# Optimization experiments

Measured on AMD Instinct MI355X. Metric: run time of the kernel, lower is better.

## Reference

```python
import jax, jax.numpy as jnp
import numpy as np

BETA = 0.25


def setup_inputs() -> dict:
    key = jax.random.key(0)
    k1, k2 = jax.random.split(key)
    x = jax.random.normal(k1, (4, 4096, 256), dtype=jnp.float32)
    emb = jax.random.normal(k2, (8192, 256), dtype=jnp.float32)
    return {"x": x, "emb": emb}


def reference(x, emb):
    B, C, D = x.shape
    xf = x.reshape(-1, D)  # [B*C, D]
    # squared euclidean distances (argmin-equivalent to torch.cdist p=2)
    # dist2[i, n] = ||xf_i||^2 - 2 xf_i . e_n + ||e_n||^2
    dist2 = (
        jnp.sum(xf * xf, axis=-1, keepdims=True)
        - 2.0 * jnp.einsum("td,nd->tn", xf, emb)
        + jnp.sum(emb * emb, axis=-1)[None, :]
    )  # [B*C, N]
    idx = jnp.argmin(dist2, axis=-1)  # [B*C]
    quant = emb[idx]  # [B*C, D]
    commitment_loss = jnp.mean((jax.lax.stop_gradient(quant) - xf) ** 2)
    codebook_loss = jnp.mean((quant - jax.lax.stop_gradient(xf)) ** 2)
    quantize_loss = codebook_loss + BETA * commitment_loss
    # straight-through estimator
    quant_out = xf + jax.lax.stop_gradient(quant - xf)
    quant_out = quant_out.reshape(B, C, D)
    indices = idx.reshape(B, C)
    return quant_out, quantize_loss, indices
```

## Files before the change

### kernel.cpp

```cpp
#include <hip/hip_runtime.h>
#include <stdint.h>

#define T_ROWS 16384
#define D_DIM  256
#define N_CODES 8192
#define NSPLIT 4
#define NS (N_CODES / NSPLIT)
#define NCHUNK (NS / 128)
#define NITER (NCHUNK * 8)

typedef _Float16 h8v __attribute__((ext_vector_type(8)));
typedef float f4v __attribute__((ext_vector_type(4)));
typedef unsigned short u16;
typedef unsigned int u32;
typedef unsigned long long u64;

typedef const __attribute__((address_space(1))) uint32_t* as1_t;
typedef __attribute__((address_space(3))) uint32_t* as3_t;

__device__ __forceinline__ void gload_lds16(const void* g, void* l) {
    __builtin_amdgcn_global_load_lds((as1_t)(uintptr_t)g, (as3_t)(uintptr_t)l, 16, 0, 0);
}
__device__ __forceinline__ u32 umin32(u32 a, u32 b) { return a < b ? a : b; }
__device__ __forceinline__ u32 umax32(u32 a, u32 b) { return a > b ? a : b; }

__global__ void k_prep_emb(const float* __restrict__ emb, u16* __restrict__ Ef,
                           float* __restrict__ enormP) {
    int wv = threadIdx.x >> 6, lane = threadIdx.x & 63;
    int row = blockIdx.x * 4 + wv;
    float4 v = *reinterpret_cast<const float4*>(emb + (size_t)row * D_DIM + lane * 4);
    float s = v.x * v.x + v.y * v.y + v.z * v.z + v.w * v.w;
    ushort4 h;
    { _Float16 t0=(_Float16)v.x,t1=(_Float16)v.y,t2=(_Float16)v.z,t3=(_Float16)v.w;
      h.x=*reinterpret_cast<u16*>(&t0); h.y=*reinterpret_cast<u16*>(&t1);
      h.z=*reinterpret_cast<u16*>(&t2); h.w=*reinterpret_cast<u16*>(&t3); }
    reinterpret_cast<ushort4*>(Ef + (size_t)row * D_DIM)[lane] = h;
#pragma unroll
    for (int off = 32; off; off >>= 1) s += __shfl_xor(s, off, 64);
    if (lane == 0) enormP[row] = s + 1024.0f;
}

__global__ __launch_bounds__(256, 2)
void k_main_mfma(const float* __restrict__ x, const u16* __restrict__ Ef,
                 const float* __restrict__ enormP, u32* __restrict__ cand) {
    __shared__ u16 Bs[4][4096];

    const int tid = threadIdx.x;
    const int lane = tid & 63;
    const int w = tid >> 6;
    const int c15 = lane & 15, grp = lane >> 4;
    const int m0 = (int)(blockIdx.x >> 2) * 128;
    const int split = (int)(blockIdx.x & 3);
    const int nbase = split * NS;

    int boff[8];
#pragma unroll
    for (int ni = 0; ni < 8; ++ni) {
        int r = ni * 16 + c15;
        boff[ni] = (r * 64 + grp * 16) ^ (((r >> 1) & 3) << 4);
    }
    const int srow = tid >> 2;
    const int kkb = ((tid & 3) ^ ((srow >> 1) & 3)) * 8;

    h8v a[2][8];
#pragma unroll
    for (int mi = 0; mi < 2; ++mi)
#pragma unroll
        for (int ks = 0; ks < 8; ++ks) {
            const float* p = x + (size_t)(m0 + w * 32 + mi * 16 + c15) * D_DIM + ks * 32 + grp * 8;
            float4 u0 = *reinterpret_cast<const float4*>(p);
            float4 u1 = *reinterpret_cast<const float4*>(p + 4);
            h8v av;
            av[0] = (_Float16)u0.x; av[1] = (_Float16)u0.y;
            av[2] = (_Float16)u0.z; av[3] = (_Float16)u0.w;
            av[4] = (_Float16)u1.x; av[5] = (_Float16)u1.y;
            av[6] = (_Float16)u1.z; av[7] = (_Float16)u1.w;
            a[mi][ks] = av;
        }

    auto stageB = [&](int buf, int it) {
        const int nc = it >> 3, ks = it & 7;
        const u16* src = Ef + (size_t)(nbase + nc * 128 + srow) * D_DIM + ks * 32 + kkb;
        gload_lds16(src, (char*)Bs + buf * 8192 + tid * 16);
        gload_lds16(src + 64 * D_DIM, (char*)Bs + buf * 8192 + 4096 + tid * 16);
    };

    u32 b1[8], b2[8];
#pragma unroll
    for (int l = 0; l < 8; ++l) { b1[l] = 0xFFFFFFFFu; b2[l] = 0xFFFFFFFFu; }

    stageB(0, 0);
    stageB(1, 1);
    stageB(2, 2);
    asm volatile("s_waitcnt vmcnt(4)\n\ts_barrier" ::: "memory");

    h8v bcur[8], bnxt[8];
#pragma unroll
    for (int ni = 0; ni < 8; ++ni)
        bcur[ni] = *reinterpret_cast<const h8v*>((const char*)Bs + boff[ni]);

    f4v acc[2][8];
    float en[8];

    auto do_step = [&](int it, int ks, h8v (&bc)[8], h8v (&bn)[8]) {
        asm volatile("s_waitcnt vmcnt(2)\n\ts_barrier" ::: "memory");
        {
            int it3 = it + 3;
            if (it3 > NITER - 1) it3 = NITER - 1;
            stageB((it + 3) & 3, it3);
        }
        if (ks == 0) {
            const int nc = it >> 3;
#pragma unroll
            for (int ni = 0; ni < 8; ++ni)
                en[ni] = enormP[nbase + nc * 128 + ni * 16 + c15];
        }
        {
            const char* bsb = (const char*)Bs + ((it + 1) & 3) * 8192;
#pragma unroll
            for (int ni = 0; ni < 8; ++ni)
                bn[ni] = *reinterpret_cast<const h8v*>(bsb + boff[ni]);
        }
        __builtin_amdgcn_s_setprio(1);
#pragma unroll
        for (int mi = 0; mi < 2; ++mi)
#pragma unroll
            for (int ni = 0; ni < 8; ++ni)
                acc[mi][ni] = __builtin_amdgcn_mfma_f32_16x16x32_f16(
                    a[mi][ks], bc[ni], acc[mi][ni], 0, 0, 0);
        __builtin_amdgcn_s_setprio(0);

        if (ks == 7) {
            const int nc = it >> 3;
#pragma unroll
            for (int mi = 0; mi < 2; ++mi)
#pragma unroll
                for (int r = 0; r < 4; ++r) {
                    const int l = mi * 4 + r;
                    u32 kmin = 0xFFFFFFFFu;
#pragma unroll
                    for (int ni = 0; ni < 8; ++ni) {
                        float s = fmaf(-2.0f, acc[mi][ni][r], en[ni]);
                        u32 k = (__float_as_uint(s) & 0xFFFFF800u)
                              | (u32)(nc * 128 + ni * 16 + c15);
                        kmin = umin32(kmin, k);
                    }
                    b2[l] = umin32(b2[l], umax32(b1[l], kmin));
                    b1[l] = umin32(b1[l], kmin);
                }
        }
    };

    for (int nc = 0; nc < NCHUNK; ++nc) {
#pragma unroll
        for (int mi = 0; mi < 2; ++mi)
#pragma unroll
            for (int ni = 0; ni < 8; ++ni) acc[mi][ni] = f4v{0.f, 0.f, 0.f, 0.f};

#pragma unroll
        for (int kp = 0; kp < 4; ++kp) {
            do_step(nc * 8 + kp * 2 + 0, kp * 2 + 0, bcur, bnxt);
            do_step(nc * 8 + kp * 2 + 1, kp * 2 + 1, bnxt, bcur);
        }
    }

#pragma unroll
    for (int l = 0; l < 8; ++l) {
#pragma unroll
        for (int off = 1; off < 16; off <<= 1) {
            u32 o1 = __shfl_xor(b1[l], off, 64);
            u32 o2 = __shfl_xor(b2[l], off, 64);
            b2[l] = umin32(umax32(b1[l], o1), umin32(b2[l], o2));
            b1[l] = umin32(b1[l], o1);
        }
    }
    if (c15 == 0) {
#pragma unroll
        for (int mi = 0; mi < 2; ++mi)
#pragma unroll
            for (int r = 0; r < 4; ++r) {
                const int l = mi * 4 + r;
                const int grow = m0 + w * 32 + mi * 16 + grp * 4 + r;
                cand[grow * 8 + split * 2 + 0] = (u32)nbase + (b1[l] & 0x7FFu);
                cand[grow * 8 + split * 2 + 1] = (u32)nbase + (b2[l] & 0x7FFu);
            }
    }
}

__global__ void k_refine(const float* __restrict__ x, const float* __restrict__ emb,
                         const u32* __restrict__ cand, float* __restrict__ out,
                         double* __restrict__ partials) {
    const int tid = threadIdx.x;
    const int wv = tid >> 6, lane = tid & 63;
    const int row = blockIdx.x * 4 + wv;
    const int cslot = lane >> 3, sub = lane & 7;
    int idx = (int)cand[row * 8 + cslot];
    double d = 0.0;
#pragma unroll
    for (int j = 0; j < 8; ++j) {
        float4 xv = *reinterpret_cast<const float4*>(x + (size_t)row * D_DIM + sub * 32 + j * 4);
        float4 ev = *reinterpret_cast<const float4*>(emb + (size_t)idx * D_DIM + sub * 32 + j * 4);
        double d0 = (double)xv.x - (double)ev.x;
        double d1 = (double)xv.y - (double)ev.y;
        double d2 = (double)xv.z - (double)ev.z;
        double d3 = (double)xv.w - (double)ev.w;
        d += d0 * d0 + d1 * d1 + d2 * d2 + d3 * d3;
    }
#pragma unroll
    for (int off = 1; off < 8; off <<= 1) d += __shfl_xor(d, off, 64);
#pragma unroll
    for (int off = 8; off < 64; off <<= 1) {
        double od = __shfl_xor(d, off, 64);
        int oi = __shfl_xor(idx, off, 64);
        bool better = (od < d) || (od == d && oi < idx);
        d = better ? od : d;
        idx = better ? oi : idx;
    }
    if (lane == 0) {
        out[(size_t)T_ROWS * D_DIM + 1 + row] = (float)idx;
        partials[row] = d;
    }
    float4 e = *reinterpret_cast<const float4*>(emb + (size_t)idx * D_DIM + lane * 4);
    *reinterpret_cast<float4*>(out + (size_t)row * D_DIM + lane * 4) = e;
}

__global__ void k_loss_d(const double* __restrict__ partials, float* __restrict__ out) {
    double s = 0.0;
    const int t = threadIdx.x;
#pragma unroll
    for (int i = 0; i < 64; ++i) s += partials[t + 256 * i];
#pragma unroll
    for (int off = 32; off; off >>= 1) s += __shfl_xor(s, off, 64);
    __shared__ double sm[4];
    const int wv = t >> 6, lane = t & 63;
    if (lane == 0) sm[wv] = s;
    __syncthreads();
    if (t == 0) {
        const double tot = sm[0] + sm[1] + sm[2] + sm[3];
        out[(size_t)T_ROWS * D_DIM] = (float)(1.25 * tot / (double)((size_t)T_ROWS * D_DIM));
    }
}

__global__ void k_enorm(const float* __restrict__ emb, float* __restrict__ enorm) {
    int wave = threadIdx.x >> 6, lane = threadIdx.x & 63;
    int row = blockIdx.x * 4 + wave;
    float4 v = *reinterpret_cast<const float4*>(emb + (size_t)row * D_DIM + lane * 4);
    float s = v.x * v.x + v.y * v.y + v.z * v.z + v.w * v.w;
#pragma unroll
    for (int off = 32; off; off >>= 1) s += __shfl_xor(s, off, 64);
    if (lane == 0) enorm[row] = s;
}

__global__ void k_init(u64* __restrict__ keys) {
    keys[blockIdx.x * blockDim.x + threadIdx.x] = ~0ull;
}

__global__ __launch_bounds__(256, 2)
void k_main_fp32(const float* __restrict__ x, const float* __restrict__ emb,
                 const float* __restrict__ enorm, u64* __restrict__ keys) {
    __shared__ float Xs[32][128];
    __shared__ float Es[32][128];
    __shared__ u64 red[128][16];

    const int tid = threadIdx.x;
    const int tx = tid & 15, ty = tid >> 4;
    const int m0 = (blockIdx.x >> 2) * 128;
    const int nbase = (blockIdx.x & 3) * (N_CODES / 4);

    float best[8];
    int bidx[8];
#pragma unroll
    for (int r = 0; r < 8; ++r) { best[r] = 3.4e38f; bidx[r] = 0; }

    for (int nc = 0; nc < (N_CODES / 4) / 128; ++nc) {
        const int n0 = nbase + nc * 128;
        float acc[8][8] = {};
        for (int k0 = 0; k0 < D_DIM; k0 += 32) {
            __syncthreads();
            {
                const int m = tid & 127, q = tid >> 7;
#pragma unroll
                for (int i = 0; i < 4; ++i) {
                    const int k4 = q * 4 + i * 8;
                    float4 v = *reinterpret_cast<const float4*>(
                        x + (size_t)(m0 + m) * D_DIM + k0 + k4);
                    Xs[k4 + 0][m] = v.x; Xs[k4 + 1][m] = v.y;
                    Xs[k4 + 2][m] = v.z; Xs[k4 + 3][m] = v.w;
                }
            }
            {
                const int kq = (tid & 7) * 4, nrow = tid >> 3;
#pragma unroll
                for (int i = 0; i < 4; ++i) {
                    const int n = i * 32 + nrow;
                    float4 v = *reinterpret_cast<const float4*>(
                        emb + (size_t)(n0 + n) * D_DIM + k0 + kq);
                    const int c = n ^ kq;
                    Es[kq + 0][c] = v.x; Es[kq + 1][c] = v.y;
                    Es[kq + 2][c] = v.z; Es[kq + 3][c] = v.w;
                }
            }
            __syncthreads();
#pragma unroll
            for (int kkx = 0; kkx < 32; ++kkx) {
                const int swz = kkx & 28;
                float4 xa = *reinterpret_cast<const float4*>(&Xs[kkx][ty * 4]);
                float4 xb = *reinterpret_cast<const float4*>(&Xs[kkx][64 + ty * 4]);
                const int cb = (tx * 4) ^ swz;
                float4 ea = *reinterpret_cast<const float4*>(&Es[kkx][cb]);
                float4 eb = *reinterpret_cast<const float4*>(&Es[kkx][64 + cb]);
                float xr[8] = {xa.x, xa.y, xa.z, xa.w, xb.x, xb.y, xb.z, xb.w};
                float ec[8] = {ea.x, ea.y, ea.z, ea.w, eb.x, eb.y, eb.z, eb.w};
#pragma unroll
                for (int r = 0; r < 8; ++r)
#pragma unroll
                    for (int c = 0; c < 8; ++c)
                        acc[r][c] = fmaf(xr[r], ec[c], acc[r][c]);
            }
        }
#pragma unroll
        for (int c = 0; c < 8; ++c) {
            const int ncol = n0 + ((c < 4) ? (tx * 4 + c) : (64 + tx * 4 + (c - 4)));
            const float en = enorm[ncol];
#pragma unroll
            for (int r = 0; r < 8; ++r) {
                const float score = fmaf(-2.0f, acc[r][c], en);
                if (score < best[r]) { best[r] = score; bidx[r] = ncol; }
            }
        }
    }
#pragma unroll
    for (int r = 0; r < 8; ++r) {
        const int row = (r < 4) ? (ty * 4 + r) : (64 + ty * 4 + (r - 4));
        unsigned u = __float_as_uint(best[r]);
        u = (u & 0x80000000u) ? ~u : (u | 0x80000000u);
        red[row][tx] = ((u64)u << 32) | (unsigned)bidx[r];
    }
    __syncthreads();
    if (tid < 128) {
        u64 k = red[tid][0];
#pragma unroll
        for (int t = 1; t < 16; ++t) { u64 v = red[tid][t]; k = (v < k) ? v : k; }
        atomicMin(&keys[m0 + tid], k);
    }
}

__global__ void k_out_fb(const float* __restrict__ x, const float* __restrict__ emb,
                         const u64* __restrict__ keys, float* __restrict__ out,
                         float* __restrict__ partials) {
    const int tid = threadIdx.x;
    const int m0 = blockIdx.x * 64;
    __shared__ int idx_s[64];
    if (tid < 64) {
        const u32 idx = (u32)keys[m0 + tid];
        idx_s[tid] = (int)idx;
        out[(size_t)T_ROWS * D_DIM + 1 + m0 + tid] = (float)idx;
    }
    __syncthreads();
    const int wave = tid >> 6, lane = tid & 63;
    float loss = 0.f;
#pragma unroll
    for (int i = 0; i < 16; ++i) {
        const int r = i * 4 + wave;
        const int row = m0 + r;
        const int idx = idx_s[r];
        float4 e  = *reinterpret_cast<const float4*>(emb + (size_t)idx * D_DIM + lane * 4);
        float4 xv = *reinterpret_cast<const float4*>(x + (size_t)row * D_DIM + lane * 4);
        *reinterpret_cast<float4*>(out + (size_t)row * D_DIM + lane * 4) = e;
        const float dx = e.x - xv.x, dy = e.y - xv.y, dz = e.z - xv.z, dw = e.w - xv.w;
        loss += dx * dx + dy * dy + dz * dz + dw * dw;
    }
#pragma unroll
    for (int off = 32; off; off >>= 1) loss += __shfl_xor(loss, off, 64);
    __shared__ float wl[4];
    if (lane == 0) wl[wave] = loss;
    __syncthreads();
    if (tid == 0) partials[blockIdx.x] = wl[0] + wl[1] + wl[2] + wl[3];
}

__global__ void k_loss_f(const float* __restrict__ partials, float* __restrict__ out) {
    double s = (double)partials[threadIdx.x];
#pragma unroll
    for (int off = 32; off; off >>= 1) s += __shfl_xor(s, off, 64);
    __shared__ double sm[4];
    const int wave = threadIdx.x >> 6, lane = threadIdx.x & 63;
    if (lane == 0) sm[wave] = s;
    __syncthreads();
    if (threadIdx.x == 0) {
        const double tot = sm[0] + sm[1] + sm[2] + sm[3];
        out[(size_t)T_ROWS * D_DIM] = (float)(1.25 * tot / (double)((size_t)T_ROWS * D_DIM));
    }
}

extern "C" void kernel_launch(void* const* d_in, const int* in_sizes, int n_in,
                              void* d_out, int out_size, void* d_ws, size_t ws_size,
                              hipStream_t stream) {
    const float* x = (const float*)d_in[0];
    const float* emb = (const float*)d_in[1];
    float* out = (float*)d_out;
    char* ws = (char*)d_ws;

    const size_t NEED = 4867072ull;
    if (ws_size >= NEED) {
        u16* Ef = (u16*)(ws + 0);
        float* enormP = (float*)(ws + 4194304);
        u32* cand = (u32*)(ws + 4227072);
        double* partials = (double*)(ws + 4751360);

        k_prep_emb<<<N_CODES / 4, 256, 0, stream>>>(emb, Ef, enormP);
        k_main_mfma<<<(T_ROWS / 128) * NSPLIT, 256, 0, stream>>>(x, Ef, enormP, cand);
        k_refine<<<T_ROWS / 4, 256, 0, stream>>>(x, emb, cand, out, partials);
        k_loss_d<<<1, 256, 0, stream>>>(partials, out);
    } else {
        float* enorm = (float*)(ws + 0);
        u64* keys = (u64*)(ws + 32768);
        float* partials = (float*)(ws + 163840);

        k_enorm<<<N_CODES / 4, 256, 0, stream>>>(emb, enorm);
        k_init<<<T_ROWS / 256, 256, 0, stream>>>(keys);
        k_main_fp32<<<(T_ROWS / 128) * 4, 256, 0, stream>>>(x, emb, enorm, keys);
        k_out_fb<<<T_ROWS / 64, 256, 0, stream>>>(x, emb, keys, out, partials);
        k_loss_f<<<1, 256, 0, stream>>>(partials, out);
    }
}
```

Measured before the change: 119.2 us.

## Deepen LDS ring to 8 buffers and process two k-steps per barrier

Doubles the shared-memory ring for codebook tiles to 8 buffers and prefetches four stages ahead. Each barrier now covers two k-steps, halving the number of barriers. The register double-buffering of B fragments is dropped in favour of loading both k-step fragments from LDS just before their MFMAs. This is meant to reduce sync overhead and give global loads more latency slack, but it doubles LDS use per block and exposes LDS read latency before the MFMAs.

```diff
diff --git a/kernel.cpp b/kernel.cpp
--- a/kernel.cpp
+++ b/kernel.cpp
@@ -43,7 +43,7 @@
 __global__ __launch_bounds__(256, 2)
 void k_main_mfma(const float* __restrict__ x, const u16* __restrict__ Ef,
                  const float* __restrict__ enormP, u32* __restrict__ cand) {
-    __shared__ u16 Bs[4][4096];
+    __shared__ u16 Bs[8][4096];
 
     const int tid = threadIdx.x;
     const int lane = tid & 63;
@@ -92,75 +92,78 @@
     stageB(0, 0);
     stageB(1, 1);
     stageB(2, 2);
+    stageB(3, 3);
     asm volatile("s_waitcnt vmcnt(4)\n\ts_barrier" ::: "memory");
-
-    h8v bcur[8], bnxt[8];
-#pragma unroll
-    for (int ni = 0; ni < 8; ++ni)
-        bcur[ni] = *reinterpret_cast<const h8v*>((const char*)Bs + boff[ni]);
 
     f4v acc[2][8];
     float en[8];
 
-    auto do_step = [&](int it, int ks, h8v (&bc)[8], h8v (&bn)[8]) {
-        asm volatile("s_waitcnt vmcnt(2)\n\ts_barrier" ::: "memory");
-        {
-            int it3 = it + 3;
-            if (it3 > NITER - 1) it3 = NITER - 1;
-            stageB((it + 3) & 3, it3);
-        }
-        if (ks == 0) {
-            const int nc = it >> 3;
-#pragma unroll
-            for (int ni = 0; ni < 8; ++ni)
-                en[ni] = enormP[nbase + nc * 128 + ni * 16 + c15];
-        }
-        {
-            const char* bsb = (const char*)Bs + ((it + 1) & 3) * 8192;
-#pragma unroll
-            for (int ni = 0; ni < 8; ++ni)
-                bn[ni] = *reinterpret_cast<const h8v*>(bsb + boff[ni]);
-        }
-        __builtin_amdgcn_s_setprio(1);
+    for (int nc = 0; nc < NCHUNK; ++nc) {
+#pragma unroll
+        for (int ni = 0; ni < 8; ++ni)
+            en[ni] = enormP[nbase + nc * 128 + ni * 16 + c15];
 #pragma unroll
         for (int mi = 0; mi < 2; ++mi)
 #pragma unroll
-            for (int ni = 0; ni < 8; ++ni)
-                acc[mi][ni] = __builtin_amdgcn_mfma_f32_16x16x32_f16(
-                    a[mi][ks], bc[ni], acc[mi][ni], 0, 0, 0);
-        __builtin_amdgcn_s_setprio(0);
-
-        if (ks == 7) {
-            const int nc = it >> 3;
+            for (int ni = 0; ni < 8; ++ni) acc[mi][ni] = f4v{0.f, 0.f, 0.f, 0.f};
+
+#pragma unroll
+        for (int kp = 0; kp < 4; ++kp) {
+            const int it = nc * 8 + kp * 2;
+
+            {
+                int t4 = it + 4; if (t4 > NITER - 1) t4 = NITER - 1;
+                int t5 = it + 5; if (t5 > NITER - 1) t5 = NITER - 1;
+                stageB((it + 4) & 7, t4);
+                stageB((it + 5) & 7, t5);
+            }
+
+            h8v b0[8], b1v[8];
+            {
+                const char* p0 = (const char*)Bs + ((it) & 7) * 8192;
+                const char* p1 = (const char*)Bs + ((it + 1) & 7) * 8192;
+#pragma unroll
+                for (int ni = 0; ni < 8; ++ni) b0[ni] = *reinterpret_cast<const h8v*>(p0 + boff[ni]);
+#pragma unroll
+                for (int ni = 0; ni < 8; ++ni) b1v[ni] = *reinterpret_cast<const h8v*>(p1 + boff[ni]);
+            }
+
+            __builtin_amdgcn_s_setprio(1);
 #pragma unroll
             for (int mi = 0; mi < 2; ++mi)
 #pragma unroll
-                for (int r = 0; r < 4; ++r) {
-                    const int l = mi * 4 + r;
-                    u32 kmin = 0xFFFFFFFFu;
-#pragma unroll
-                    for (int ni = 0; ni < 8; ++ni) {
-                        float s = fmaf(-2.0f, acc[mi][ni][r], en[ni]);
-                        u32 k = (__float_as_uint(s) & 0xFFFFF800u)
-                              | (u32)(nc * 128 + ni * 16 + c15);
-                        kmin = umin32(kmin, k);
+                for (int ni = 0; ni < 8; ++ni)
+                    acc[mi][ni] = __builtin_amdgcn_mfma_f32_16x16x32_f16(
+                        a[mi][kp * 2], b0[ni], acc[mi][ni], 0, 0, 0);
+#pragma unroll
+            for (int mi = 0; mi < 2; ++mi)
+#pragma unroll
+                for (int ni = 0; ni < 8; ++ni)
+                    acc[mi][ni] = __builtin_amdgcn_mfma_f32_16x16x32_f16(
+                        a[mi][kp * 2 + 1], b1v[ni], acc[mi][ni], 0, 0, 0);
+            __builtin_amdgcn_s_setprio(0);
+
+            if (kp == 3) {
+#pragma unroll
+                for (int mi = 0; mi < 2; ++mi)
+#pragma unroll
+                    for (int r = 0; r < 4; ++r) {
+                        const int l = mi * 4 + r;
+                        u32 kmin = 0xFFFFFFFFu;
+#pragma unroll
+                        for (int ni = 0; ni < 8; ++ni) {
+                            float s = fmaf(-2.0f, acc[mi][ni][r], en[ni]);
+                            u32 k = (__float_as_uint(s) & 0xFFFFF800u)
+                                  | (u32)(nc * 128 + ni * 16 + c15);
+                            kmin = umin32(kmin, k);
+                        }
+                        b2[l] = umin32(b2[l], umax32(b1[l], kmin));
+                        b1[l] = umin32(b1[l], kmin);
                     }
-                    b2[l] = umin32(b2[l], umax32(b1[l], kmin));
-                    b1[l] = umin32(b1[l], kmin);
-                }
-        }
-    };
-
-    for (int nc = 0; nc < NCHUNK; ++nc) {
-#pragma unroll
-        for (int mi = 0; mi < 2; ++mi)
-#pragma unroll
-            for (int ni = 0; ni < 8; ++ni) acc[mi][ni] = f4v{0.f, 0.f, 0.f, 0.f};
-
-#pragma unroll
-        for (int kp = 0; kp < 4; ++kp) {
-            do_step(nc * 8 + kp * 2 + 0, kp * 2 + 0, bcur, bnxt);
-            do_step(nc * 8 + kp * 2 + 1, kp * 2 + 1, bnxt, bcur);
+            }
+
+            if (!(nc == NCHUNK - 1 && kp == 3))
+                asm volatile("s_waitcnt vmcnt(4)\n\ts_barrier" ::: "memory");
         }
     }
 
```

Result: slower. 123.1 us (+3.3%).
